# Optimization experiments

Hardware: AMD Instinct MI355X
Metric: run time of the kernel (lower is better)

Reference implementation:

```python
import jax, jax.numpy as jnp
import numpy as np


def setup_inputs() -> dict:
    key = jax.random.key(0)
    k1, k2 = jax.random.split(key)
    B, C, M, N = 4, 3, 4096, 8192
    query = jax.random.normal(k1, (B, C, M), dtype=jnp.float32)
    points = jax.random.normal(k2, (B, C, N), dtype=jnp.float32)
    return {"k": 16, "query": query, "points": points}


def reference(k, query, points):
    # query: BxCxM, points: BxCxN  (trans=True path of original module)
    q = jnp.swapaxes(query, 1, 2)   # BxMxC
    p = jnp.swapaxes(points, 1, 2)  # BxNxC
    # squared L2 distances (FAISS GpuIndexFlatL2): BxMxN
    q2 = jnp.sum(q * q, axis=-1, keepdims=True)           # BxMx1
    p2 = jnp.sum(p * p, axis=-1)[:, None, :]              # Bx1xN
    dist = q2 + p2 - 2.0 * jnp.einsum('bmc,bnc->bmn', q, p)
    # k smallest distances, sorted ascending (FAISS sorts results)
    _, index_batch = jax.lax.top_k(-dist, k)              # BxMxK int32
    index_batch = index_batch.astype(jnp.int64) if index_batch.dtype != jnp.int64 else index_batch
    # gather neighbor coordinates: points BxCxN, idx BxMxK -> BxCxMxK
    neighbor_points = jax.vmap(lambda pts, idx: pts[:, idx])(points, index_batch)
    return neighbor_points, index_batch
```

## Files before the change

kernel.cpp:

```cpp
#include <hip/hip_runtime.h>
#include <stdint.h>

#define BQ 4
#define CC 3
#define MM 4096
#define NN 8192
#define KK 16
#define NP_OFF (BQ*CC*MM*KK)
#define BLOCK 512
#define RPW 8
#define GROUPS 2
#define QTS 4
#define ROWS (GROUPS*RPW)
#define CHUNK 1024
#define NCH (NN/CHUNK)
#define CST (CHUNK/64)
#define QST (CST/QTS)
#define EPSD 1e-4f

__device__ __forceinline__ float rfl(float x) {
    return __uint_as_float((unsigned)__builtin_amdgcn_readfirstlane((int)__float_as_uint(x)));
}
__device__ __forceinline__ unsigned mapf(float f) {
    unsigned u = __float_as_uint(f);
    return (u & 0x80000000u) ? ~u : (u | 0x80000000u);
}
__device__ __forceinline__ float unmapf(unsigned u) {
    unsigned b = (u & 0x80000000u) ? (u & 0x7fffffffu) : ~u;
    return __uint_as_float(b);
}

__global__ __launch_bounds__(BLOCK, 8) void knn_kernel(
    const float* __restrict__ query,
    const float* __restrict__ points,
    float* __restrict__ out)
{
    __shared__ float4 pts[2][CHUNK];
    __shared__ unsigned aux[ROWS][64];
    __shared__ unsigned scnt[ROWS];
    __shared__ unsigned rcbits[ROWS];

    const int tid  = threadIdx.x;
    const int lane = tid & 63;
    const int wv   = tid >> 6;
    const int g    = wv >> 2;
    const int qt   = wv & 3;
    const int bid  = blockIdx.x;
    const int b    = bid >> 8;
    const int rb   = (bid & 255) * ROWS;

    const float* pb = points + b * (CC * NN);
    const float* qb = query  + b * (CC * MM);

    ((unsigned*)aux)[tid]       = 0u;
    ((unsigned*)aux)[tid + 512] = 0u;
    if (tid < ROWS) scnt[tid] = 0u;

    float qx[RPW], qy[RPW], qz[RPW], dm[RPW];
    #pragma unroll
    for (int r = 0; r < RPW; ++r) {
        int m = rb + g * RPW + r;
        qx[r] = rfl(qb[m]);
        qy[r] = rfl(qb[MM + m]);
        qz[r] = rfl(qb[2*MM + m]);
        dm[r] = -__builtin_inff();
    }

    auto stage = [&](int ch, int bi) {
        #pragma unroll
        for (int i = 0; i < CHUNK / BLOCK; ++i) {
            int ii = i * BLOCK + tid;
            int n  = ch * CHUNK + ii;
            float px = pb[n], py = pb[NN + n], pz = pb[2*NN + n];
            float p2 = __fadd_rn(__fadd_rn(__fmul_rn(px,px), __fmul_rn(py,py)),
                                 __fmul_rn(pz,pz));
            pts[bi][ii] = make_float4(px, py, pz, -0.5f * p2);
        }
    };

    auto comp1 = [&](int bi) {
        #pragma unroll
        for (int t = 0; t < QST; ++t) {
            float4 P = pts[bi][((qt * QST + t) << 6) + lane];
            #pragma unroll
            for (int r = 0; r < RPW; ++r) {
                float dotf = __builtin_fmaf(qz[r], P.z,
                              __builtin_fmaf(qy[r], P.y,
                               __builtin_fmaf(qx[r], P.x, P.w)));
                dm[r] = fmaxf(dm[r], dotf);
            }
        }
    };

    stage(0, 0);
    #pragma unroll 1
    for (int ch = 0; ch < NCH; ch += 2) {
        __syncthreads();
        if (ch + 1 < NCH) stage(ch + 1, 1);
        comp1(0);
        __syncthreads();
        if (ch + 2 < NCH) stage(ch + 2, 0);
        if (ch + 1 < NCH) comp1(1);
    }

    #pragma unroll
    for (int r = 0; r < RPW; ++r)
        atomicMax(&aux[g*RPW + r][lane], mapf(dm[r]));
    __syncthreads();

    #pragma unroll
    for (int rr = 0; rr < 2; ++rr) {
        int row = 2*wv + rr;
        unsigned v = aux[row][lane];
        #pragma unroll
        for (int k = 2; k <= 64; k <<= 1) {
            #pragma unroll
            for (int j = k >> 1; j > 0; j >>= 1) {
                unsigned o = __shfl_xor(v, j, 64);
                bool keepmin = (((lane & j) == 0) == ((lane & k) == 0));
                v = keepmin ? (v < o ? v : o) : (v > o ? v : o);
            }
        }
        unsigned tb = __shfl(v, 48, 64);
        if (lane == 0) rcbits[row] = __float_as_uint(unmapf(tb) - EPSD);
    }
    __syncthreads();

    float rc[RPW];
    #pragma unroll
    for (int r = 0; r < RPW; ++r)
        rc[r] = rfl(__uint_as_float(rcbits[g*RPW + r]));

    auto comp2 = [&](int ch, int bi) {
        #pragma unroll
        for (int t = 0; t < QST; ++t) {
            int st = qt * QST + t;
            float4 P = pts[bi][(st << 6) + lane];
            unsigned n = (unsigned)(ch * CHUNK + (st << 6) + lane);
            #pragma unroll
            for (int r = 0; r < RPW; ++r) {
                float dotf = __builtin_fmaf(qz[r], P.z,
                              __builtin_fmaf(qy[r], P.y,
                               __builtin_fmaf(qx[r], P.x, P.w)));
                if (dotf >= rc[r]) {
                    unsigned pos = atomicAdd(&scnt[g*RPW + r], 1u);
                    if (pos < 64u) aux[g*RPW + r][pos] = n;
                }
            }
        }
    };

    stage(0, 0);
    #pragma unroll 1
    for (int ch = 0; ch < NCH; ch += 2) {
        __syncthreads();
        if (ch + 1 < NCH) stage(ch + 1, 1);
        comp2(ch, 0);
        __syncthreads();
        if (ch + 2 < NCH) stage(ch + 2, 0);
        if (ch + 1 < NCH) comp2(ch + 1, 1);
    }
    __syncthreads();

    #pragma unroll
    for (int rr = 0; rr < 2; ++rr) {
        int row = 2*wv + rr;
        int m   = rb + row;
        float ex = rfl(qb[m]);
        float ey = rfl(qb[MM + m]);
        float ez = rfl(qb[2*MM + m]);
        float eq2 = rfl(__fadd_rn(__fadd_rn(__fmul_rn(ex,ex), __fmul_rn(ey,ey)),
                                  __fmul_rn(ez,ez)));
        unsigned c = scnt[row]; if (c > 64u) c = 64u;
        unsigned kb = 0xffffffffu, id = 0xffffffffu;
        if (lane < (int)c) {
            id = aux[row][lane];
            float px = pb[id], py = pb[NN + id], pz = pb[2*NN + id];
            float p2 = __fadd_rn(__fadd_rn(__fmul_rn(px,px), __fmul_rn(py,py)),
                                 __fmul_rn(pz,pz));
            float dot = __builtin_fmaf(ez, pz,
                         __builtin_fmaf(ey, py, __fmul_rn(ex, px)));
            float d = __fsub_rn(__fadd_rn(eq2, p2), __fmul_rn(2.0f, dot));
            unsigned fb = __float_as_uint(d);
            kb = (fb & 0x80000000u) ? ~fb : (fb | 0x80000000u);
        }
        #pragma unroll
        for (int k = 2; k <= 64; k <<= 1) {
            #pragma unroll
            for (int j = k >> 1; j > 0; j >>= 1) {
                unsigned ok = __shfl_xor(kb, j, 64);
                unsigned oi = __shfl_xor(id, j, 64);
                bool takeMin  = (((lane & j) == 0) == ((lane & k) == 0));
                bool selfLess = (kb < ok) || (kb == ok && id < oi);
                if (selfLess != takeMin) { kb = ok; id = oi; }
            }
        }
        if (lane < KK) {
            int oi = (int)id;
            out[NP_OFF + (b * MM + m) * KK + lane] = (float)oi;
            out[((b * CC + 0) * MM + m) * KK + lane] = pb[oi];
            out[((b * CC + 1) * MM + m) * KK + lane] = pb[NN + oi];
            out[((b * CC + 2) * MM + m) * KK + lane] = pb[2*NN + oi];
        }
    }
}

extern "C" void kernel_launch(void* const* d_in, const int* in_sizes, int n_in,
                              void* d_out, int out_size, void* d_ws, size_t ws_size,
                              hipStream_t stream) {
    const float* query  = (const float*)d_in[1];
    const float* points = (const float*)d_in[2];
    float* out = (float*)d_out;
    dim3 grid(BQ * (MM / ROWS));
    dim3 block(BLOCK);
    knn_kernel<<<grid, block, 0, stream>>>(query, points, out);
}
```

Measured before the change: 105.4 us.

## Compute KNN distance scores with split-bf16 MFMA and pre-packed operand tiles

Adds a pack kernel that splits query and point coordinates into hi/lo bf16 parts and lays them out as MFMA operand fragments in the workspace. The main kernel then computes the dot-product-minus-half-norm scores with 32x32x16 bf16 matrix instructions instead of scalar FMAs, and stages point tiles into LDS with direct global-to-LDS loads. Each block now handles 32 query rows. The threshold margin is widened to absorb the approximation error of the bf16 split, and exact fp32 distances are still recomputed for the final candidates. The cost is an extra kernel launch and workspace traffic, plus a risk that the candidate filter drops a true neighbour if the error bound is too loose.

```diff
diff --git a/kernel.cpp b/kernel.cpp
--- a/kernel.cpp
+++ b/kernel.cpp
@@ -8,15 +8,20 @@
 #define KK 16
 #define NP_OFF (BQ*CC*MM*KK)
 #define BLOCK 512
-#define RPW 8
-#define GROUPS 2
-#define QTS 4
-#define ROWS (GROUPS*RPW)
+#define ROWS 32
 #define CHUNK 1024
 #define NCH (NN/CHUNK)
-#define CST (CHUNK/64)
-#define QST (CST/QTS)
-#define EPSD 1e-4f
+#define EPSA 4e-3f
+
+typedef __attribute__((ext_vector_type(8)))  short   short8;
+typedef __attribute__((ext_vector_type(8)))  __bf16  bf16x8;
+typedef __attribute__((ext_vector_type(16))) float   f32x16;
+typedef unsigned int u32;
+typedef unsigned short u16;
+
+#define BT_PER_BATCH 256
+#define AT_PER_BATCH 128
+#define A_OFF (BQ*BT_PER_BATCH*64)
 
 __device__ __forceinline__ float rfl(float x) {
     return __uint_as_float((unsigned)__builtin_amdgcn_readfirstlane((int)__float_as_uint(x)));
@@ -29,13 +34,69 @@
     unsigned b = (u & 0x80000000u) ? (u & 0x7fffffffu) : ~u;
     return __uint_as_float(b);
 }
-
-__global__ __launch_bounds__(BLOCK, 8) void knn_kernel(
+__device__ __forceinline__ u16 bfh(float f) {
+    unsigned u = __float_as_uint(f);
+    return (u16)((u + 0x7fffu + ((u >> 16) & 1u)) >> 16);
+}
+__device__ __forceinline__ float bff(u16 h) {
+    return __uint_as_float(((unsigned)h) << 16);
+}
+
+__device__ __forceinline__ f32x16 mfma3216(short8 a, short8 b, f32x16 c) {
+    return __builtin_amdgcn_mfma_f32_32x32x16_bf16(
+        __builtin_bit_cast(bf16x8, a), __builtin_bit_cast(bf16x8, b), c, 0, 0, 0);
+}
+
+__device__ __forceinline__ void gl_lds16(const void* g, void* l) {
+    __builtin_amdgcn_global_load_lds(
+        (const __attribute__((address_space(1))) u32*)g,
+        (__attribute__((address_space(3))) u32*)l, 16, 0, 0);
+}
+
+__global__ void pack_kernel(const float* __restrict__ query,
+                            const float* __restrict__ points,
+                            short8* __restrict__ ws)
+{
+    const int lane = threadIdx.x;
+    const int bid  = blockIdx.x;
+    const int hi   = lane >> 5;
+    const int j    = lane & 31;
+    short8 v = {0,0,0,0,0,0,0,0};
+    if (bid < BQ*BT_PER_BATCH) {
+        const int b = bid >> 8, tile = bid & 255;
+        const int n = tile*32 + j;
+        const float* pb = points + b*(CC*NN);
+        float px = pb[n], py = pb[NN+n], pz = pb[2*NN+n];
+        float pw = -0.5f*(px*px + py*py + pz*pz);
+        u16 xh=bfh(px), yh=bfh(py), zh=bfh(pz), wh=bfh(pw);
+        u16 xl=bfh(px-bff(xh)), yl=bfh(py-bff(yh)), zl=bfh(pz-bff(zh)), wl=bfh(pw-bff(wh));
+        if (hi == 0) { v[0]=(short)xh; v[1]=(short)xh; v[2]=(short)xl; v[3]=(short)yh;
+                       v[4]=(short)zl; v[5]=(short)wh; v[6]=(short)wl; v[7]=0; }
+        else         { v[0]=(short)yh; v[1]=(short)yl; v[2]=(short)zh; v[3]=(short)zh; }
+        ws[bid*64 + lane] = v;
+    } else {
+        const int t2 = bid - BQ*BT_PER_BATCH;
+        const int b = t2 >> 7, rt = t2 & 127;
+        const int m = rt*32 + j;
+        const float* qb = query + b*(CC*MM);
+        float qx = qb[m], qy = qb[MM+m], qz = qb[2*MM+m];
+        u16 xh=bfh(qx), yh=bfh(qy), zh=bfh(qz);
+        u16 xl=bfh(qx-bff(xh)), yl=bfh(qy-bff(yh)), zl=bfh(qz-bff(zh));
+        const u16 ONE = 0x3F80u;
+        if (hi == 0) { v[0]=(short)xh; v[1]=(short)xl; v[2]=(short)xh; v[3]=(short)yh;
+                       v[4]=(short)zh; v[5]=(short)ONE; v[6]=(short)ONE; v[7]=0; }
+        else         { v[0]=(short)yl; v[1]=(short)yh; v[2]=(short)zh; v[3]=(short)zl; }
+        ws[A_OFF + t2*64 + lane] = v;
+    }
+}
+
+__global__ __launch_bounds__(BLOCK, 4) void knn_kernel(
     const float* __restrict__ query,
     const float* __restrict__ points,
+    const short8* __restrict__ ws,
     float* __restrict__ out)
 {
-    __shared__ float4 pts[2][CHUNK];
+    __shared__ short8 bpk[2][2048];
     __shared__ unsigned aux[ROWS][64];
     __shared__ unsigned scnt[ROWS];
     __shared__ unsigned rcbits[ROWS];
@@ -43,51 +104,50 @@
     const int tid  = threadIdx.x;
     const int lane = tid & 63;
     const int wv   = tid >> 6;
-    const int g    = wv >> 2;
-    const int qt   = wv & 3;
+    const int col  = lane & 31;
+    const int hi4  = (lane >> 5) << 2;
     const int bid  = blockIdx.x;
-    const int b    = bid >> 8;
-    const int rb   = (bid & 255) * ROWS;
-
-    const float* pb = points + b * (CC * NN);
-    const float* qb = query  + b * (CC * MM);
-
-    ((unsigned*)aux)[tid]       = 0u;
-    ((unsigned*)aux)[tid + 512] = 0u;
+    const int b    = bid >> 7;
+    const int rt   = bid & 127;
+    const int rb   = rt * 32;
+
+    const float* pb = points + b*(CC*NN);
+    const float* qb = query  + b*(CC*MM);
+
+    #pragma unroll
+    for (int i = 0; i < 4; ++i) ((unsigned*)aux)[i*BLOCK + tid] = 0u;
     if (tid < ROWS) scnt[tid] = 0u;
 
-    float qx[RPW], qy[RPW], qz[RPW], dm[RPW];
-    #pragma unroll
-    for (int r = 0; r < RPW; ++r) {
-        int m = rb + g * RPW + r;
-        qx[r] = rfl(qb[m]);
-        qy[r] = rfl(qb[MM + m]);
-        qz[r] = rfl(qb[2*MM + m]);
-        dm[r] = -__builtin_inff();
-    }
+    const short8 af = ws[A_OFF + (b*AT_PER_BATCH + rt)*64 + lane];
+    const f32x16 zf = {0.f,0.f,0.f,0.f,0.f,0.f,0.f,0.f,
+                       0.f,0.f,0.f,0.f,0.f,0.f,0.f,0.f};
+
+    float rm0[16], rm1[16];
+    #pragma unroll
+    for (int j = 0; j < 16; ++j) { rm0[j] = -__builtin_inff(); rm1[j] = -__builtin_inff(); }
+
+    const short8* Bb = ws + (size_t)b * (BT_PER_BATCH*64);
 
     auto stage = [&](int ch, int bi) {
         #pragma unroll
-        for (int i = 0; i < CHUNK / BLOCK; ++i) {
-            int ii = i * BLOCK + tid;
-            int n  = ch * CHUNK + ii;
-            float px = pb[n], py = pb[NN + n], pz = pb[2*NN + n];
-            float p2 = __fadd_rn(__fadd_rn(__fmul_rn(px,px), __fmul_rn(py,py)),
-                                 __fmul_rn(pz,pz));
-            pts[bi][ii] = make_float4(px, py, pz, -0.5f * p2);
+        for (int i = 0; i < 4; ++i) {
+            int idx = i*BLOCK + tid;
+            gl_lds16(&Bb[ch*2048 + idx], &bpk[bi][idx]);
         }
     };
 
     auto comp1 = [&](int bi) {
         #pragma unroll
-        for (int t = 0; t < QST; ++t) {
-            float4 P = pts[bi][((qt * QST + t) << 6) + lane];
-            #pragma unroll
-            for (int r = 0; r < RPW; ++r) {
-                float dotf = __builtin_fmaf(qz[r], P.z,
-                              __builtin_fmaf(qy[r], P.y,
-                               __builtin_fmaf(qx[r], P.x, P.w)));
-                dm[r] = fmaxf(dm[r], dotf);
+        for (int p = 0; p < 2; ++p) {
+            short8 b0 = bpk[bi][(wv*4 + p)*64 + lane];
+            short8 b1 = bpk[bi][(wv*4 + p + 2)*64 + lane];
+            f32x16 d0 = mfma3216(af, b0, zf);
+            f32x16 d1 = mfma3216(af, b1, zf);
+            #pragma unroll
+            for (int j = 0; j < 16; ++j) {
+                float t = fmaxf(d0[j], d1[j]);
+                if (p == 0) rm0[j] = fmaxf(rm0[j], t);
+                else        rm1[j] = fmaxf(rm1[j], t);
             }
         }
     };
@@ -104,53 +164,63 @@
     }
 
     #pragma unroll
-    for (int r = 0; r < RPW; ++r)
-        atomicMax(&aux[g*RPW + r][lane], mapf(dm[r]));
+    for (int j = 0; j < 16; ++j) {
+        int row = ((j & 3) + 8*(j >> 2)) + hi4;
+        atomicMax(&aux[row][col],      mapf(rm0[j]));
+        atomicMax(&aux[row][col + 32], mapf(rm1[j]));
+    }
     __syncthreads();
-
-    #pragma unroll
-    for (int rr = 0; rr < 2; ++rr) {
-        int row = 2*wv + rr;
+    stage(0, 0);
+
+    #pragma unroll
+    for (int rr = 0; rr < 4; ++rr) {
+        int row = wv*4 + rr;
         unsigned v = aux[row][lane];
         #pragma unroll
         for (int k = 2; k <= 64; k <<= 1) {
             #pragma unroll
-            for (int j = k >> 1; j > 0; j >>= 1) {
-                unsigned o = __shfl_xor(v, j, 64);
-                bool keepmin = (((lane & j) == 0) == ((lane & k) == 0));
+            for (int jj = k >> 1; jj > 0; jj >>= 1) {
+                unsigned o = __shfl_xor(v, jj, 64);
+                bool keepmin = (((lane & jj) == 0) == ((lane & k) == 0));
                 v = keepmin ? (v < o ? v : o) : (v > o ? v : o);
             }
         }
         unsigned tb = __shfl(v, 48, 64);
-        if (lane == 0) rcbits[row] = __float_as_uint(unmapf(tb) - EPSD);
+        if (lane == 0) rcbits[row] = __float_as_uint(unmapf(tb) - EPSA);
     }
     __syncthreads();
 
-    float rc[RPW];
-    #pragma unroll
-    for (int r = 0; r < RPW; ++r)
-        rc[r] = rfl(__uint_as_float(rcbits[g*RPW + r]));
+    float rcv[16];
+    #pragma unroll
+    for (int j = 0; j < 16; ++j)
+        rcv[j] = __uint_as_float(rcbits[((j & 3) + 8*(j >> 2)) + hi4]);
 
     auto comp2 = [&](int ch, int bi) {
         #pragma unroll
-        for (int t = 0; t < QST; ++t) {
-            int st = qt * QST + t;
-            float4 P = pts[bi][(st << 6) + lane];
-            unsigned n = (unsigned)(ch * CHUNK + (st << 6) + lane);
-            #pragma unroll
-            for (int r = 0; r < RPW; ++r) {
-                float dotf = __builtin_fmaf(qz[r], P.z,
-                              __builtin_fmaf(qy[r], P.y,
-                               __builtin_fmaf(qx[r], P.x, P.w)));
-                if (dotf >= rc[r]) {
-                    unsigned pos = atomicAdd(&scnt[g*RPW + r], 1u);
-                    if (pos < 64u) aux[g*RPW + r][pos] = n;
+        for (int p = 0; p < 2; ++p) {
+            short8 b0 = bpk[bi][(wv*4 + p)*64 + lane];
+            short8 b1 = bpk[bi][(wv*4 + p + 2)*64 + lane];
+            f32x16 d0 = mfma3216(af, b0, zf);
+            f32x16 d1 = mfma3216(af, b1, zf);
+            unsigned n0 = (unsigned)(ch*CHUNK + (wv*4 + p)*32 + col);
+            #pragma unroll
+            for (int j = 0; j < 16; ++j) {
+                float t = fmaxf(d0[j], d1[j]);
+                if (t >= rcv[j]) {
+                    int row = ((j & 3) + 8*(j >> 2)) + hi4;
+                    if (d0[j] >= rcv[j]) {
+                        unsigned pos = atomicAdd(&scnt[row], 1u);
+                        if (pos < 64u) aux[row][pos] = n0;
+                    }
+                    if (d1[j] >= rcv[j]) {
+                        unsigned pos = atomicAdd(&scnt[row], 1u);
+                        if (pos < 64u) aux[row][pos] = n0 + 64u;
+                    }
                 }
             }
         }
     };
 
-    stage(0, 0);
     #pragma unroll 1
     for (int ch = 0; ch < NCH; ch += 2) {
         __syncthreads();
@@ -162,9 +232,9 @@
     }
     __syncthreads();
 
-    #pragma unroll
-    for (int rr = 0; rr < 2; ++rr) {
-        int row = 2*wv + rr;
+    #pragma unroll 1
+    for (int rr = 0; rr < 4; ++rr) {
+        int row = wv*4 + rr;
         int m   = rb + row;
         float ex = rfl(qb[m]);
         float ey = rfl(qb[MM + m]);
@@ -211,7 +281,10 @@
     const float* query  = (const float*)d_in[1];
     const float* points = (const float*)d_in[2];
     float* out = (float*)d_out;
-    dim3 grid(BQ * (MM / ROWS));
-    dim3 block(BLOCK);
-    knn_kernel<<<grid, block, 0, stream>>>(query, points, out);
-}
+    short8* ws = (short8*)d_ws;
+
+    pack_kernel<<<dim3(BQ*BT_PER_BATCH + BQ*AT_PER_BATCH), dim3(64), 0, stream>>>(
+        query, points, ws);
+    knn_kernel<<<dim3(BQ * (MM / ROWS)), dim3(BLOCK), 0, stream>>>(
+        query, points, ws, out);
+}
```

After: 105.0 us. About the same (-0.3%).
